# Performance work log

Measured on AMD Instinct MI355X. Metric: run time of the kernel, lower is better.

## Reference

```python
import jax, jax.numpy as jnp
import numpy as np

N_X = 20000      # bessel x-grid
N_ELL = 48       # sparse tabulated multipoles
N_K = 1024       # k quadrature points
N_TAU = 600      # conformal-time samples
K_PIVOT = 0.05


def fast_interp(x, xmin, xmax, ytab):
    """Uniform-grid linear interpolation (tools.fast_interp). ytab: [Nx]."""
    n = ytab.shape[0]
    pos = jnp.clip((x - xmin) / (xmax - xmin) * (n - 1), 0.0, n - 1.0)
    i0 = jnp.clip(jnp.floor(pos).astype(jnp.int32), 0, n - 2)
    w = pos - i0
    return ytab[i0] * (1.0 - w) + ytab[i0 + 1] * w


def setup_inputs() -> dict:
    key = jax.random.key(0)
    ks = jax.random.split(key, 8)
    k = jnp.logspace(-4.0, 0.0, N_K, dtype=jnp.float32)           # Mpc^-1
    tau = jnp.linspace(50.0, 14000.0, N_TAU, dtype=jnp.float32)    # Mpc
    tau0 = jnp.asarray(14100.0, dtype=jnp.float32)
    bessel_x_tab = jnp.linspace(0.0, 15000.0, N_X, dtype=jnp.float32)
    mk = lambda kk, sh, s: (s * jax.random.normal(kk, sh, dtype=jnp.float32))
    return {
        "k": k,
        "tau": tau,
        "tau0": tau0,
        "S0": mk(ks[0], (N_K, N_TAU), 1e-2),
        "S1": mk(ks[1], (N_K, N_TAU), 1e-2),
        "S2": mk(ks[2], (N_K, N_TAU), 1e-2),
        "SE": mk(ks[3], (N_K, N_TAU), 1e-2),
        "bessel_x_tab": bessel_x_tab,
        "phi0_tab": mk(ks[4], (N_X, N_ELL), 1e-1),
        "phi1_tab": mk(ks[5], (N_X, N_ELL), 1e-1),
        "phi2_tab": mk(ks[6], (N_X, N_ELL), 1e-1),
        "eps_tab": mk(ks[7], (N_X, N_ELL), 1e-1),
        "A_s": jnp.asarray(2.1e-9, dtype=jnp.float32),
        "n_s": jnp.asarray(0.965, dtype=jnp.float32),
    }


def reference(k, tau, tau0, S0, S1, S2, SE, bessel_x_tab,
              phi0_tab, phi1_tab, phi2_tab, eps_tab, A_s, n_s):
    xmin = bessel_x_tab[0]
    xmax = bessel_x_tab[-1]
    # radial argument x = k * (tau0 - tau): [K, T]
    x = k[:, None] * (tau0 - tau)[None, :]

    def one_ell(p0, p1, p2, pe):
        # lookup phi0/phi1/phi2/epsilon at every (k, tau), fuse with sources
        srcT = (S0 * fast_interp(x, xmin, xmax, p0)
                + S1 * fast_interp(x, xmin, xmax, p1)
                + S2 * fast_interp(x, xmin, xmax, p2))
        Tl = jnp.trapezoid(srcT, tau, axis=-1)                       # [K]
        El = jnp.trapezoid(SE * fast_interp(x, xmin, xmax, pe), tau, axis=-1)
        return Tl, El

    # vmap over the tabulated-ell axis (columns of the Bessel tables)
    Tl, El = jax.vmap(one_ell, in_axes=(1, 1, 1, 1))(
        phi0_tab, phi1_tab, phi2_tab, eps_tab)                       # [L, K]

    # primordial curvature spectrum P_R(k) = A_s (k/k_p)^(n_s-1) * 2 pi^2 / k^3
    P_R = A_s * (k / K_PIVOT) ** (n_s - 1.0) * (2.0 * jnp.pi ** 2 / k ** 3)
    w = k * k * P_R                                                   # [K]
    c = 2.0 / jnp.pi
    ClTT = c * jnp.trapezoid(w * Tl * Tl, k, axis=-1)                 # [L]
    ClEE = c * jnp.trapezoid(w * El * El, k, axis=-1)
    ClTE = c * jnp.trapezoid(w * Tl * El, k, axis=-1)
    return jnp.stack([ClTT, ClEE, ClTE], axis=0)                      # [3, L]
```

## Files before the change

kernel.cpp:

```cpp
#include <hip/hip_runtime.h>
#include <math.h>

#define N_X   20000
#define N_ELL 48
#define N_K   1024
#define N_TAU 600
#define SPLIT 4
#define CHUNK (N_TAU / SPLIT)
#define ROWB  (N_ELL * 16)
#define KCH   4
#define PADN  160

__device__ __forceinline__ unsigned int pack_half2(float lo, float hi) {
    _Float16 l = (_Float16)lo, h = (_Float16)hi;
    unsigned short lu = __builtin_bit_cast(unsigned short, l);
    unsigned short hu = __builtin_bit_cast(unsigned short, h);
    return (unsigned int)lu | ((unsigned int)hu << 16);
}
__device__ __forceinline__ float fdot2(unsigned int a, unsigned int b, float c) {
    float d;
    asm("v_dot2_f32_f16 %0, %1, %2, %3" : "=v"(d) : "v"(a), "v"(b), "v"(c));
    return d;
}

__global__ __launch_bounds__(256) void repack_kernel(
    const float* __restrict__ p0, const float* __restrict__ p1,
    const float* __restrict__ p2, const float* __restrict__ pe,
    uint4* __restrict__ P, float* __restrict__ out)
{
    if (blockIdx.x == 0 && threadIdx.x < 3 * N_ELL) out[threadIdx.x] = 0.0f;
    const int total = N_X * N_ELL;
    for (int idx = blockIdx.x * blockDim.x + threadIdx.x; idx < total;
         idx += gridDim.x * blockDim.x) {
        int x = idx / N_ELL;
        int e = idx - x * N_ELL;
        int xn = (x < N_X - 1) ? x + 1 : x;
        int a = x * N_ELL + e, b = xn * N_ELL + e;
        uint4 v;
        v.x = pack_half2(p0[a], p0[b]);
        v.y = pack_half2(p1[a], p1[b]);
        v.z = pack_half2(p2[a], p2[b]);
        v.w = pack_half2(pe[a], pe[b]);
        P[idx] = v;
    }
}

__global__ __launch_bounds__(256) void tl_el_packed(
    const float* __restrict__ k, const float* __restrict__ tau,
    const float* __restrict__ tau0p,
    const float* __restrict__ S0, const float* __restrict__ S1,
    const float* __restrict__ S2, const float* __restrict__ SE,
    const float* __restrict__ bx, const uint4* __restrict__ P,
    float* __restrict__ Tlp, float* __restrict__ Elp)
{
    const int bid  = blockIdx.x;
    const int part = bid & (SPLIT - 1);
    const int kidx = (N_K - 1) - (bid >> 2);
    const int t0   = part * CHUNK;
    const int tid  = threadIdx.x;
    const int wave = tid >> 6;
    const int lane = tid & 63;
    const int ell  = (lane < N_ELL) ? lane : (N_ELL - 1);

    __shared__ unsigned int off_s[PADN];
    __shared__ uint4        WT_s[PADN];
    __shared__ float        redT[4][N_ELL];
    __shared__ float        redE[4][N_ELL];

    const float kk    = k[kidx];
    const float tau0  = tau0p[0];
    const float xmin  = bx[0];
    const float xmax  = bx[N_X - 1];
    const float scale = (float)(N_X - 1) / (xmax - xmin);

    if (tid < CHUNK) {
        int t = t0 + tid;
        float tt = tau[t];
        float tp = (t > 0)         ? tau[t - 1] : tt;
        float tn = (t < N_TAU - 1) ? tau[t + 1] : tt;
        float wt = 0.5f * (tn - tp);
        float x   = kk * (tau0 - tt);
        float pos = (x - xmin) * scale;
        pos = fminf(fmaxf(pos, 0.0f), (float)(N_X - 1));
        int i0 = (int)pos;
        if (i0 > N_X - 2) i0 = N_X - 2;
        float w  = pos - (float)i0;
        float om = 1.0f - w;
        size_t sb = (size_t)kidx * N_TAU + t;
        float s0 = wt * S0[sb], s1 = wt * S1[sb];
        float s2 = wt * S2[sb], se = wt * SE[sb];
        uint4 w2;
        w2.x = pack_half2(s0 * om, s0 * w);
        w2.y = pack_half2(s1 * om, s1 * w);
        w2.z = pack_half2(s2 * om, s2 * w);
        w2.w = pack_half2(se * om, se * w);
        WT_s[tid]  = w2;
        off_s[tid] = (unsigned int)i0 * (unsigned int)ROWB;
    } else if (tid < PADN) {
        uint4 z4; z4.x = z4.y = z4.z = z4.w = 0u;
        WT_s[tid]  = z4;
        off_s[tid] = 0u;
    }
    __syncthreads();

    const char* Pb = (const char*)P;
    const unsigned int elloff = (unsigned int)ell * 16u;
    float aT0 = 0.0f, aT1 = 0.0f, aT2 = 0.0f, aE = 0.0f;

    uint4 A[8], B[8];

#define ISSUE(BUF, G)                                                      \
    _Pragma("unroll")                                                      \
    for (int m = 0; m < 8; ++m) {                                          \
        unsigned int voff = off_s[wave + 4 * m + 32 * (G)] + elloff;       \
        BUF[m] = *(const uint4*)(Pb + voff);                               \
    }

#define CONSUME(BUF, G)                                                    \
    _Pragma("unroll")                                                      \
    for (int m = 0; m < 8; ++m) {                                          \
        int idx = wave + 4 * m + 32 * (G);                                 \
        uint4 w2 = WT_s[idx];                                              \
        aT0 = fdot2(BUF[m].x, w2.x, aT0);                                  \
        aT1 = fdot2(BUF[m].y, w2.y, aT1);                                  \
        aT2 = fdot2(BUF[m].z, w2.z, aT2);                                  \
        aE  = fdot2(BUF[m].w, w2.w, aE);                                   \
    }

#define SB __builtin_amdgcn_sched_barrier(0)

    ISSUE(A, 0); SB;
    ISSUE(B, 1); SB;
    CONSUME(A, 0); ISSUE(A, 2); SB;
    CONSUME(B, 1); ISSUE(B, 3); SB;
    CONSUME(A, 2); ISSUE(A, 4); SB;
    CONSUME(B, 3); SB;
    CONSUME(A, 4);

#undef ISSUE
#undef CONSUME
#undef SB

    float accT = (aT0 + aT1) + aT2;

    if (lane < N_ELL) { redT[wave][lane] = accT; redE[wave][lane] = aE; }
    __syncthreads();
    if (tid < N_ELL) {
        float sT = (redT[0][tid] + redT[1][tid]) + (redT[2][tid] + redT[3][tid]);
        float sE = (redE[0][tid] + redE[1][tid]) + (redE[2][tid] + redE[3][tid]);
        Tlp[((size_t)part * N_ELL + tid) * N_K + kidx] = sT;
        Elp[((size_t)part * N_ELL + tid) * N_K + kidx] = sE;
    }
}

__global__ __launch_bounds__(256) void tl_el_kernel(
    const float* __restrict__ k, const float* __restrict__ tau,
    const float* __restrict__ tau0p,
    const float* __restrict__ S0, const float* __restrict__ S1,
    const float* __restrict__ S2, const float* __restrict__ SE,
    const float* __restrict__ bx,
    const float* __restrict__ p0, const float* __restrict__ p1,
    const float* __restrict__ p2, const float* __restrict__ pe,
    float* __restrict__ Tl, float* __restrict__ El)
{
    const int kidx = blockIdx.x;
    const int tid  = threadIdx.x;
    const int wave = tid >> 6;
    const int lane = tid & 63;
    const int ell  = (lane < N_ELL) ? lane : (N_ELL - 1);

    const float kk    = k[kidx];
    const float tau0  = tau0p[0];
    const float xmin  = bx[0];
    const float xmax  = bx[N_X - 1];
    const float scale = (float)(N_X - 1) / (xmax - xmin);

    const float* Srow0 = S0 + (size_t)kidx * N_TAU;
    const float* Srow1 = S1 + (size_t)kidx * N_TAU;
    const float* Srow2 = S2 + (size_t)kidx * N_TAU;
    const float* SrowE = SE + (size_t)kidx * N_TAU;

    float accT = 0.0f, accE = 0.0f;

    for (int t = wave; t < N_TAU; t += 4) {
        float tt    = tau[t];
        float tprev = (t > 0)         ? tau[t - 1] : tt;
        float tnext = (t < N_TAU - 1) ? tau[t + 1] : tt;
        float wt    = 0.5f * (tnext - tprev);

        float x   = kk * (tau0 - tt);
        float pos = (x - xmin) * scale;
        pos = fminf(fmaxf(pos, 0.0f), (float)(N_X - 1));
        int i0 = (int)floorf(pos);
        if (i0 > N_X - 2) i0 = N_X - 2;
        float w = pos - (float)i0;

        int base = i0 * N_ELL + ell;
        float y00 = p0[base], y01 = p0[base + N_ELL];
        float y10 = p1[base], y11 = p1[base + N_ELL];
        float y20 = p2[base], y21 = p2[base + N_ELL];
        float ye0 = pe[base], ye1 = pe[base + N_ELL];

        float a0 = fmaf(w, y01 - y00, y00);
        float a1 = fmaf(w, y11 - y10, y10);
        float a2 = fmaf(w, y21 - y20, y20);
        float ae = fmaf(w, ye1 - ye0, ye0);

        float s0 = Srow0[t], s1 = Srow1[t], s2 = Srow2[t], se = SrowE[t];

        float srcT = s0 * a0 + s1 * a1 + s2 * a2;
        accT = fmaf(wt, srcT, accT);
        accE = fmaf(wt, se * ae, accE);
    }

    __shared__ float redT[4][N_ELL];
    __shared__ float redE[4][N_ELL];
    if (lane < N_ELL) { redT[wave][lane] = accT; redE[wave][lane] = accE; }
    __syncthreads();
    if (tid < N_ELL) {
        float sT = (redT[0][tid] + redT[1][tid]) + (redT[2][tid] + redT[3][tid]);
        float sE = (redE[0][tid] + redE[1][tid]) + (redE[2][tid] + redE[3][tid]);
        Tl[tid * N_K + kidx] = sT;
        El[tid * N_K + kidx] = sE;
    }
}

__global__ __launch_bounds__(256) void cl_kernel2(
    const float* __restrict__ k,
    const float* __restrict__ Asp, const float* __restrict__ nsp,
    const float* __restrict__ Tlp, const float* __restrict__ Elp,
    int nparts, float* __restrict__ out)
{
    const int ell   = blockIdx.x;
    const int chunk = blockIdx.y;
    const int tid   = threadIdx.x;
    const int i     = chunk * 256 + tid;
    const float A_s = Asp[0];
    const float n_s = nsp[0];
    const float two_pi2 = 2.0f * (float)M_PI * (float)M_PI;

    float kv    = k[i];
    float kprev = (i > 0)       ? k[i - 1] : kv;
    float knext = (i < N_K - 1) ? k[i + 1] : kv;
    float dkw   = 0.5f * (knext - kprev);
    float Pw    = A_s * powf(kv / 0.05f, n_s - 1.0f) * two_pi2 / kv;
    float ww    = dkw * Pw;

    float tl = 0.0f, el = 0.0f;
    for (int p = 0; p < nparts; ++p) {
        tl += Tlp[((size_t)p * N_ELL + ell) * N_K + i];
        el += Elp[((size_t)p * N_ELL + ell) * N_K + i];
    }
    float aTT = ww * tl * tl;
    float aEE = ww * el * el;
    float aTE = ww * tl * el;

    for (int off = 32; off > 0; off >>= 1) {
        aTT += __shfl_down(aTT, off, 64);
        aEE += __shfl_down(aEE, off, 64);
        aTE += __shfl_down(aTE, off, 64);
    }
    __shared__ float red[3][4];
    const int wave = tid >> 6, lane = tid & 63;
    if (lane == 0) { red[0][wave] = aTT; red[1][wave] = aEE; red[2][wave] = aTE; }
    __syncthreads();
    if (tid == 0) {
        const float c = 2.0f / (float)M_PI;
        atomicAdd(&out[0 * N_ELL + ell],
                  c * ((red[0][0] + red[0][1]) + (red[0][2] + red[0][3])));
        atomicAdd(&out[1 * N_ELL + ell],
                  c * ((red[1][0] + red[1][1]) + (red[1][2] + red[1][3])));
        atomicAdd(&out[2 * N_ELL + ell],
                  c * ((red[2][0] + red[2][1]) + (red[2][2] + red[2][3])));
    }
}

extern "C" void kernel_launch(void* const* d_in, const int* in_sizes, int n_in,
                              void* d_out, int out_size, void* d_ws, size_t ws_size,
                              hipStream_t stream) {
    const float* k    = (const float*)d_in[0];
    const float* tau  = (const float*)d_in[1];
    const float* tau0 = (const float*)d_in[2];
    const float* S0   = (const float*)d_in[3];
    const float* S1   = (const float*)d_in[4];
    const float* S2   = (const float*)d_in[5];
    const float* SE   = (const float*)d_in[6];
    const float* bx   = (const float*)d_in[7];
    const float* p0   = (const float*)d_in[8];
    const float* p1   = (const float*)d_in[9];
    const float* p2   = (const float*)d_in[10];
    const float* pe   = (const float*)d_in[11];
    const float* A_s  = (const float*)d_in[12];
    const float* n_s  = (const float*)d_in[13];
    float* out = (float*)d_out;

    const size_t P_bytes    = (size_t)N_X * N_ELL * sizeof(uint4);
    const size_t part_bytes = (size_t)SPLIT * N_ELL * N_K * sizeof(float);

    if (ws_size >= P_bytes + 2 * part_bytes) {
        uint4* P   = (uint4*)d_ws;
        float* Tlp = (float*)((char*)d_ws + P_bytes);
        float* Elp = (float*)((char*)d_ws + P_bytes + part_bytes);

        repack_kernel<<<(N_X * N_ELL + 255) / 256, 256, 0, stream>>>(
            p0, p1, p2, pe, P, out);
        tl_el_packed<<<N_K * SPLIT, 256, 0, stream>>>(k, tau, tau0, S0, S1, S2, SE, bx,
                                                      P, Tlp, Elp);
        cl_kernel2<<<dim3(N_ELL, KCH), 256, 0, stream>>>(k, A_s, n_s, Tlp, Elp,
                                                         SPLIT, out);
    } else {
        float* Tl = (float*)d_ws;
        float* El = Tl + (size_t)N_ELL * N_K;
        hipMemsetAsync(out, 0, 3 * N_ELL * sizeof(float), stream);
        tl_el_kernel<<<N_K, 256, 0, stream>>>(k, tau, tau0, S0, S1, S2, SE, bx,
                                              p0, p1, p2, pe, Tl, El);
        cl_kernel2<<<dim3(N_ELL, KCH), 256, 0, stream>>>(k, A_s, n_s, Tl, El, 1, out);
    }
}
```

Before: 129.9 us.

## Split k range: stage contiguous Bessel-table band in LDS for small k

For small k the interpolation rows of a tau chunk span a narrow contiguous band of the packed table. A new kernel copies that band (up to 60 rows) into shared memory with coalesced loads and then gathers from LDS. It falls back to global gathers when the band is wider. Large k blocks keep the prefetching global-gather kernel, now with a launch-bounds occupancy hint. This adds a second launch and about 46 KB of LDS per block in exchange for fewer scattered global reads.

```diff
diff --git a/kernel.cpp b/kernel.cpp
--- a/kernel.cpp
+++ b/kernel.cpp
@@ -1,15 +1,17 @@
 #include <hip/hip_runtime.h>
 #include <math.h>
 
-#define N_X   20000
-#define N_ELL 48
-#define N_K   1024
-#define N_TAU 600
-#define SPLIT 4
-#define CHUNK (N_TAU / SPLIT)
-#define ROWB  (N_ELL * 16)
-#define KCH   4
-#define PADN  160
+#define N_X    20000
+#define N_ELL  48
+#define N_K    1024
+#define N_TAU  600
+#define SPLIT  4
+#define CHUNK  (N_TAU / SPLIT)
+#define ROWB   (N_ELL * 16)
+#define KCH    4
+#define PADN   160
+#define KSMALL 532
+#define MAXR   60
 
 __device__ __forceinline__ unsigned int pack_half2(float lo, float hi) {
     _Float16 l = (_Float16)lo, h = (_Float16)hi;
@@ -45,34 +47,13 @@
     }
 }
 
-__global__ __launch_bounds__(256) void tl_el_packed(
-    const float* __restrict__ k, const float* __restrict__ tau,
-    const float* __restrict__ tau0p,
+__device__ __forceinline__ void build_meta(
+    int tid, int t0, int kidx, float kk, float tau0, float xmin, float scale,
+    const float* __restrict__ tau,
     const float* __restrict__ S0, const float* __restrict__ S1,
     const float* __restrict__ S2, const float* __restrict__ SE,
-    const float* __restrict__ bx, const uint4* __restrict__ P,
-    float* __restrict__ Tlp, float* __restrict__ Elp)
-{
-    const int bid  = blockIdx.x;
-    const int part = bid & (SPLIT - 1);
-    const int kidx = (N_K - 1) - (bid >> 2);
-    const int t0   = part * CHUNK;
-    const int tid  = threadIdx.x;
-    const int wave = tid >> 6;
-    const int lane = tid & 63;
-    const int ell  = (lane < N_ELL) ? lane : (N_ELL - 1);
-
-    __shared__ unsigned int off_s[PADN];
-    __shared__ uint4        WT_s[PADN];
-    __shared__ float        redT[4][N_ELL];
-    __shared__ float        redE[4][N_ELL];
-
-    const float kk    = k[kidx];
-    const float tau0  = tau0p[0];
-    const float xmin  = bx[0];
-    const float xmax  = bx[N_X - 1];
-    const float scale = (float)(N_X - 1) / (xmax - xmin);
-
+    int* row_s, uint4* WT_s)
+{
     if (tid < CHUNK) {
         int t = t0 + tid;
         float tt = tau[t];
@@ -94,13 +75,45 @@
         w2.y = pack_half2(s1 * om, s1 * w);
         w2.z = pack_half2(s2 * om, s2 * w);
         w2.w = pack_half2(se * om, se * w);
-        WT_s[tid]  = w2;
-        off_s[tid] = (unsigned int)i0 * (unsigned int)ROWB;
+        WT_s[tid] = w2;
+        row_s[tid] = i0;
     } else if (tid < PADN) {
         uint4 z4; z4.x = z4.y = z4.z = z4.w = 0u;
-        WT_s[tid]  = z4;
-        off_s[tid] = 0u;
-    }
+        WT_s[tid] = z4;
+        row_s[tid] = 0;
+    }
+}
+
+__global__ __launch_bounds__(256, 4) void tl_el_gather(
+    const float* __restrict__ k, const float* __restrict__ tau,
+    const float* __restrict__ tau0p,
+    const float* __restrict__ S0, const float* __restrict__ S1,
+    const float* __restrict__ S2, const float* __restrict__ SE,
+    const float* __restrict__ bx, const uint4* __restrict__ P,
+    float* __restrict__ Tlp, float* __restrict__ Elp)
+{
+    const int bid  = blockIdx.x;
+    const int part = bid & (SPLIT - 1);
+    const int kidx = (N_K - 1) - (bid >> 2);
+    const int t0   = part * CHUNK;
+    const int tid  = threadIdx.x;
+    const int wave = tid >> 6;
+    const int lane = tid & 63;
+    const int ell  = (lane < N_ELL) ? lane : (N_ELL - 1);
+
+    __shared__ int   row_s[PADN];
+    __shared__ uint4 WT_s[PADN];
+    __shared__ float redT[4][N_ELL];
+    __shared__ float redE[4][N_ELL];
+
+    const float kk    = k[kidx];
+    const float tau0  = tau0p[0];
+    const float xmin  = bx[0];
+    const float xmax  = bx[N_X - 1];
+    const float scale = (float)(N_X - 1) / (xmax - xmin);
+
+    build_meta(tid, t0, kidx, kk, tau0, xmin, scale, tau, S0, S1, S2, SE,
+               row_s, WT_s);
     __syncthreads();
 
     const char* Pb = (const char*)P;
@@ -112,7 +125,9 @@
 #define ISSUE(BUF, G)                                                      \
     _Pragma("unroll")                                                      \
     for (int m = 0; m < 8; ++m) {                                          \
-        unsigned int voff = off_s[wave + 4 * m + 32 * (G)] + elloff;       \
+        unsigned int voff =                                                \
+            (unsigned int)row_s[wave + 4 * m + 32 * (G)] * (unsigned int)ROWB \
+            + elloff;                                                      \
         BUF[m] = *(const uint4*)(Pb + voff);                               \
     }
 
@@ -140,6 +155,82 @@
 #undef ISSUE
 #undef CONSUME
 #undef SB
+
+    float accT = (aT0 + aT1) + aT2;
+
+    if (lane < N_ELL) { redT[wave][lane] = accT; redE[wave][lane] = aE; }
+    __syncthreads();
+    if (tid < N_ELL) {
+        float sT = (redT[0][tid] + redT[1][tid]) + (redT[2][tid] + redT[3][tid]);
+        float sE = (redE[0][tid] + redE[1][tid]) + (redE[2][tid] + redE[3][tid]);
+        Tlp[((size_t)part * N_ELL + tid) * N_K + kidx] = sT;
+        Elp[((size_t)part * N_ELL + tid) * N_K + kidx] = sE;
+    }
+}
+
+__global__ __launch_bounds__(256) void tl_el_staged(
+    const float* __restrict__ k, const float* __restrict__ tau,
+    const float* __restrict__ tau0p,
+    const float* __restrict__ S0, const float* __restrict__ S1,
+    const float* __restrict__ S2, const float* __restrict__ SE,
+    const float* __restrict__ bx, const uint4* __restrict__ P,
+    float* __restrict__ Tlp, float* __restrict__ Elp)
+{
+    const int bid  = blockIdx.x;
+    const int part = bid & (SPLIT - 1);
+    const int kidx = (KSMALL - 1) - (bid >> 2);
+    const int t0   = part * CHUNK;
+    const int tid  = threadIdx.x;
+    const int wave = tid >> 6;
+    const int lane = tid & 63;
+    const int ell  = (lane < N_ELL) ? lane : (N_ELL - 1);
+
+    __shared__ int   row_s[PADN];
+    __shared__ uint4 WT_s[PADN];
+    __shared__ uint4 band[MAXR * N_ELL];
+    __shared__ float redT[4][N_ELL];
+    __shared__ float redE[4][N_ELL];
+
+    const float kk    = k[kidx];
+    const float tau0  = tau0p[0];
+    const float xmin  = bx[0];
+    const float xmax  = bx[N_X - 1];
+    const float scale = (float)(N_X - 1) / (xmax - xmin);
+
+    build_meta(tid, t0, kidx, kk, tau0, xmin, scale, tau, S0, S1, S2, SE,
+               row_s, WT_s);
+    __syncthreads();
+
+    const int imax = row_s[0];
+    const int imin = row_s[CHUNK - 1];
+    const int nrows = imax - imin + 1;
+    float aT0 = 0.0f, aT1 = 0.0f, aT2 = 0.0f, aE = 0.0f;
+
+    if (nrows <= MAXR) {
+        const uint4* src = P + (size_t)imin * N_ELL;
+        const int nelem = nrows * N_ELL;
+        #pragma unroll 4
+        for (int j = tid; j < nelem; j += 256) band[j] = src[j];
+        __syncthreads();
+
+        for (int idx = wave; idx < CHUNK; idx += 4) {
+            uint4 pr = band[(row_s[idx] - imin) * N_ELL + ell];
+            uint4 w2 = WT_s[idx];
+            aT0 = fdot2(pr.x, w2.x, aT0);
+            aT1 = fdot2(pr.y, w2.y, aT1);
+            aT2 = fdot2(pr.z, w2.z, aT2);
+            aE  = fdot2(pr.w, w2.w, aE);
+        }
+    } else {
+        for (int idx = wave; idx < CHUNK; idx += 4) {
+            uint4 pr = P[(size_t)row_s[idx] * N_ELL + ell];
+            uint4 w2 = WT_s[idx];
+            aT0 = fdot2(pr.x, w2.x, aT0);
+            aT1 = fdot2(pr.y, w2.y, aT1);
+            aT2 = fdot2(pr.z, w2.z, aT2);
+            aE  = fdot2(pr.w, w2.w, aE);
+        }
+    }
 
     float accT = (aT0 + aT1) + aT2;
 
@@ -304,8 +395,10 @@
 
         repack_kernel<<<(N_X * N_ELL + 255) / 256, 256, 0, stream>>>(
             p0, p1, p2, pe, P, out);
-        tl_el_packed<<<N_K * SPLIT, 256, 0, stream>>>(k, tau, tau0, S0, S1, S2, SE, bx,
-                                                      P, Tlp, Elp);
+        tl_el_gather<<<(N_K - KSMALL) * SPLIT, 256, 0, stream>>>(
+            k, tau, tau0, S0, S1, S2, SE, bx, P, Tlp, Elp);
+        tl_el_staged<<<KSMALL * SPLIT, 256, 0, stream>>>(
+            k, tau, tau0, S0, S1, S2, SE, bx, P, Tlp, Elp);
         cl_kernel2<<<dim3(N_ELL, KCH), 256, 0, stream>>>(k, A_s, n_s, Tlp, Elp,
                                                          SPLIT, out);
     } else {
```

After: 135.1 us. 4.0% more time.
